# Performance work log

Measured on AMD Instinct MI355X. Metric: run time of the kernel, lower is better.

The kernel has to match this reference:

```python
import jax, jax.numpy as jnp
import numpy as np

V, B, T, H, L = 32000, 32, 128, 512, 2


def setup_inputs() -> dict:
    key = jax.random.key(0)
    k0, k1, k2, k3, k4 = jax.random.split(key, 5)
    return {
        "input_data": jax.random.randint(k0, (B, T), 0, V),
        "targets": jax.random.randint(k1, (B, T), 0, V),
        # tf.random_uniform([vocab, rnn_size], -1, 1)
        "embedding": jax.random.uniform(k2, (V, H), jnp.float32, -1.0, 1.0),
        # one fused gate weight per layer: [concat(x,h)=2H, 4H], gate order i,j,f,o
        "lstm_w": jax.random.normal(k3, (L, 2 * H, 4 * H), jnp.float32) * 0.05,
        "lstm_b": jnp.zeros((L, 4 * H), jnp.float32),
        # truncated_normal(stddev=1/sqrt(rnn_size)) approximated by normal
        "softmax_w": jax.random.normal(k4, (H, V), jnp.float32) / np.sqrt(H),
        "softmax_b": jnp.zeros((V,), jnp.float32),
    }


def _lstm_forward(x_emb, lstm_w, lstm_b):
    # x_emb: [B, T, H]; stacked BasicLSTMCell, forget_bias=0.0, zero initial state
    n_layers = lstm_w.shape[0]
    Bn, Tn, Hn = x_emb.shape
    c0 = jnp.zeros((n_layers, Bn, Hn), x_emb.dtype)
    h0 = jnp.zeros((n_layers, Bn, Hn), x_emb.dtype)

    def step(carry, x_t):
        c, h = carry
        inp = x_t  # [B, H]
        new_c, new_h = [], []
        for l in range(n_layers):  # small fixed structural loop
            gates = jnp.concatenate([inp, h[l]], axis=-1) @ lstm_w[l] + lstm_b[l]
            i, j, f, o = jnp.split(gates, 4, axis=-1)  # TF gate order
            nc = c[l] * jax.nn.sigmoid(f) + jax.nn.sigmoid(i) * jnp.tanh(j)
            nh = jnp.tanh(nc) * jax.nn.sigmoid(o)
            new_c.append(nc)
            new_h.append(nh)
            inp = nh
        return (jnp.stack(new_c), jnp.stack(new_h)), inp

    _, outs = jax.lax.scan(step, (c0, h0), jnp.swapaxes(x_emb, 0, 1))  # [T, B, H]
    return jnp.swapaxes(outs, 0, 1)  # [B, T, H]


def reference(input_data, targets, embedding, lstm_w, lstm_b, softmax_w, softmax_b):
    x = embedding[input_data]  # [B, T, H] gather
    h = _lstm_forward(x, lstm_w, lstm_b)
    logits = h.reshape(-1, h.shape[-1]) @ softmax_w + softmax_b  # [B*T, V]
    logp = jax.nn.log_softmax(logits, axis=-1)
    tflat = targets.reshape(-1)
    loss = -jnp.take_along_axis(logp, tflat[:, None], axis=1)[:, 0]  # per-example CE
    cost = jnp.mean(loss)
    return logits, cost
```

## Files before the change

### kernel.cpp

```cpp
#include <hip/hip_runtime.h>
#include <math.h>

#define VV 32000
#define BB 32
#define TT 128
#define HH 512
#define G4 2048
#define BTT 4096

typedef unsigned short u16;
typedef __attribute__((ext_vector_type(8))) short short8;
typedef __attribute__((ext_vector_type(4))) float f32x4;

static __device__ __forceinline__ float sigm(float x) { return 1.0f / (1.0f + expf(-x)); }

static __device__ __forceinline__ void bsplit(float v, u16& h, u16& l) {
    unsigned u = __float_as_uint(v);
    h = (u16)((u + 0x7FFFu + ((u >> 16) & 1u)) >> 16);
    float vh = __uint_as_float(((unsigned)h) << 16);
    unsigned u2 = __float_as_uint(v - vh);
    l = (u16)((u2 + 0x7FFFu + ((u2 >> 16) & 1u)) >> 16);
}

static __device__ __forceinline__ void gl_lds16(const void* g, void* l) {
    __builtin_amdgcn_global_load_lds(
        (const __attribute__((address_space(1))) void*)g,
        (__attribute__((address_space(3))) void*)l, 16, 0, 0);
}

__global__ void k_gather_split(const int* __restrict__ idx, const float* __restrict__ emb,
                               u16* __restrict__ hi, u16* __restrict__ lo) {
    int row = blockIdx.x;
    int e = idx[row];
    float4 v = ((const float4*)(emb + (size_t)e * HH))[threadIdx.x];
    ushort4 h4, l4;
    bsplit(v.x, h4.x, l4.x); bsplit(v.y, h4.y, l4.y);
    bsplit(v.z, h4.z, l4.z); bsplit(v.w, h4.w, l4.w);
    size_t o = (size_t)row * HH + threadIdx.x * 4;
    *(ushort4*)(hi + o) = h4;
    *(ushort4*)(lo + o) = l4;
}

__global__ void k_split4(const float* __restrict__ x, u16* __restrict__ hi,
                         u16* __restrict__ lo, int n4) {
    int i = blockIdx.x * 256 + threadIdx.x;
    if (i >= n4) return;
    float4 v = ((const float4*)x)[i];
    ushort4 h4, l4;
    bsplit(v.x, h4.x, l4.x); bsplit(v.y, h4.y, l4.y);
    bsplit(v.z, h4.z, l4.z); bsplit(v.w, h4.w, l4.w);
    *(ushort4*)(hi + (size_t)i * 4) = h4;
    *(ushort4*)(lo + (size_t)i * 4) = l4;
}

__global__ void k_zero(float* __restrict__ p, int n) {
    int i = blockIdx.x * blockDim.x + threadIdx.x;
    if (i < n) p[i] = 0.0f;
}

__global__ void k_transposeN(const float* __restrict__ src, float* __restrict__ dst, int K) {
    int gc = blockIdx.x;
    float* d = dst + (size_t)gc * K;
    for (int k = threadIdx.x; k < K; k += blockDim.x)
        d[k] = src[(size_t)k * G4 + gc];
}

__global__ __launch_bounds__(256) void k_tsplit(const float* __restrict__ src,
                                                u16* __restrict__ dhi, u16* __restrict__ dlo,
                                                int K, int N) {
    __shared__ float t[32][33];
    int kb = blockIdx.y << 5, nb = blockIdx.x << 5;
    int r = threadIdx.x >> 5, c = threadIdx.x & 31;
    #pragma unroll
    for (int it = 0; it < 4; ++it)
        t[it * 8 + r][c] = src[(size_t)(kb + it * 8 + r) * N + nb + c];
    __syncthreads();
    #pragma unroll
    for (int it = 0; it < 4; ++it) {
        int n = nb + it * 8 + r, k = kb + c;
        u16 h, l;
        bsplit(t[c][it * 8 + r], h, l);
        dhi[(size_t)n * K + k] = h;
        dlo[(size_t)n * K + k] = l;
    }
}

__global__ __launch_bounds__(256) void k_mgemm(const u16* __restrict__ Ah, const u16* __restrict__ Al,
                                               const u16* __restrict__ Bh, const u16* __restrict__ Bl,
                                               const float* __restrict__ bias, float* __restrict__ C,
                                               int N, int K) {
    __shared__ u16 lds[4][4096];
    const int tid = threadIdx.x;
    const int lane = tid & 63, wid = tid >> 6;
    const int wm = wid >> 1, wn = wid & 1;
    const int lm = lane & 15, kg = lane >> 4;
    const size_t mbase = (size_t)blockIdx.y * 128, nbase = (size_t)blockIdx.x * 128;

    f32x4 acc[4][4] = {};

    const int q = wid * 128 + lane;
    for (int k0 = 0; k0 < K; k0 += 32) {
        __syncthreads();
        #pragma unroll
        for (int i = 0; i < 2; ++i) {
            int qq = q + i * 64;
            int kgs = qq >> 7, ms = qq & 127;
            size_t ga = (mbase + ms) * K + k0 + kgs * 8;
            size_t gb = (nbase + ms) * K + k0 + kgs * 8;
            int lb_ = (wid * 2 + i) * 512;
            gl_lds16(Ah + ga, &lds[0][lb_]);
            gl_lds16(Al + ga, &lds[1][lb_]);
            gl_lds16(Bh + gb, &lds[2][lb_]);
            gl_lds16(Bl + gb, &lds[3][lb_]);
        }
        __syncthreads();

        short8 ah[4], al[4], bh[4], bl[4];
        const int abase = (kg * 128 + wm * 64 + lm) * 8;
        const int bbase = (kg * 128 + wn * 64 + lm) * 8;
        #pragma unroll
        for (int f = 0; f < 4; ++f) {
            ah[f] = *(const short8*)&lds[0][abase + f * 128];
            al[f] = *(const short8*)&lds[1][abase + f * 128];
            bh[f] = *(const short8*)&lds[2][bbase + f * 128];
            bl[f] = *(const short8*)&lds[3][bbase + f * 128];
        }
        #pragma unroll
        for (int fm = 0; fm < 4; ++fm)
            #pragma unroll
            for (int fn = 0; fn < 4; ++fn) {
                acc[fm][fn] = __builtin_amdgcn_mfma_f32_16x16x32_bf16(ah[fm], bh[fn], acc[fm][fn], 0, 0, 0);
                acc[fm][fn] = __builtin_amdgcn_mfma_f32_16x16x32_bf16(ah[fm], bl[fn], acc[fm][fn], 0, 0, 0);
                acc[fm][fn] = __builtin_amdgcn_mfma_f32_16x16x32_bf16(al[fm], bh[fn], acc[fm][fn], 0, 0, 0);
            }
    }

    float bv[4];
    #pragma unroll
    for (int fn = 0; fn < 4; ++fn) bv[fn] = bias[nbase + wn * 64 + fn * 16 + lm];
    #pragma unroll
    for (int fm = 0; fm < 4; ++fm) {
        size_t row0 = mbase + wm * 64 + fm * 16 + kg * 4;
        #pragma unroll
        for (int fn = 0; fn < 4; ++fn) {
            size_t col = nbase + wn * 64 + fn * 16 + lm;
            #pragma unroll
            for (int r = 0; r < 4; ++r)
                C[(row0 + r) * N + col] = acc[fm][fn][r] + bv[fn];
        }
    }
}

__global__ __launch_bounds__(256) void k_stepP(const float* __restrict__ wt1,
                                               const float* __restrict__ wt2,
                                               const float* __restrict__ xg1,
                                               const float* __restrict__ lb2,
                                               float* __restrict__ st,
                                               float* __restrict__ hall1,
                                               float* __restrict__ hall2,
                                               int s) {
    __shared__ float gs[512];
    float* h1buf[2] = {st, st + 16384};
    float* c1 = st + 2 * 16384;
    float* h2buf[2] = {st + 3 * 16384, st + 4 * 16384};
    float* c2 = st + 5 * 16384;
    const int tid = threadIdx.x;

    if (blockIdx.x < 128) {
        int t = s;
        if (t >= TT) return;
        const int cg = blockIdx.x >> 1;
        const int bg = blockIdx.x & 1;
        const float* hp = h1buf[t & 1];
        float* hn = h1buf[(t & 1) ^ 1];
        const int b = tid >> 4, g = (tid >> 2) & 3, ch2 = tid & 3;
        const int batch = bg * 16 + b;
        const int gc0 = g * HH + cg * 8 + ch2;
        const float4* w0 = (const float4*)(wt1 + (size_t)gc0 * HH);
        const float4* w1 = (const float4*)(wt1 + (size_t)(gc0 + 4) * HH);
        const float4* hr = (const float4*)(hp + batch * HH);
        float a0 = 0.f, a1 = 0.f;
        #pragma unroll 4
        for (int i = 0; i < HH / 4; ++i) {
            float4 h4 = hr[i], x0 = w0[i], x1 = w1[i];
            a0 += x0.x * h4.x + x0.y * h4.y + x0.z * h4.z + x0.w * h4.w;
            a1 += x1.x * h4.x + x1.y * h4.y + x1.z * h4.z + x1.w * h4.w;
        }
        size_t xrow = ((size_t)batch * TT + t) * G4;
        gs[(b * 4 + g) * 8 + ch2]     = a0 + xg1[xrow + gc0];
        gs[(b * 4 + g) * 8 + ch2 + 4] = a1 + xg1[xrow + gc0 + 4];
        __syncthreads();
        if (tid < 128) {
            int bb = tid >> 3, cc = tid & 7;
            int batch2 = bg * 16 + bb, chan = cg * 8 + cc;
            float gi = gs[(bb * 4 + 0) * 8 + cc], gj = gs[(bb * 4 + 1) * 8 + cc];
            float gf = gs[(bb * 4 + 2) * 8 + cc], go = gs[(bb * 4 + 3) * 8 + cc];
            size_t ci = (size_t)batch2 * HH + chan;
            float nc = c1[ci] * sigm(gf) + sigm(gi) * tanhf(gj);
            float nh = tanhf(nc) * sigm(go);
            c1[ci] = nc;
            hn[ci] = nh;
            hall1[((size_t)batch2 * TT + t) * HH + chan] = nh;
        }
    } else {
        int tt = s - 1;
        if (tt < 0) return;
        const int idx = blockIdx.x - 128;
        const int cg = idx >> 2;
        const int bg = idx & 3;
        const float* hp = h2buf[tt & 1];
        float* hn = h2buf[(tt & 1) ^ 1];
        const int b = tid >> 5, g = (tid >> 3) & 3, ch = tid & 7;
        const int batch = bg * 8 + b;
        const int gc = g * HH + cg * 8 + ch;
        const float4* wx = (const float4*)(wt2 + (size_t)gc * 1024);
        const float4* wh = wx + HH / 4;
        const float4* xr = (const float4*)(hall1 + ((size_t)batch * TT + tt) * HH);
        const float4* hr = (const float4*)(hp + batch * HH);
        float a = 0.f;
        #pragma unroll 4
        for (int i = 0; i < HH / 4; ++i) {
            float4 x4 = xr[i], w4 = wx[i];
            a += w4.x * x4.x + w4.y * x4.y + w4.z * x4.z + w4.w * x4.w;
        }
        #pragma unroll 4
        for (int i = 0; i < HH / 4; ++i) {
            float4 h4 = hr[i], w4 = wh[i];
            a += w4.x * h4.x + w4.y * h4.y + w4.z * h4.z + w4.w * h4.w;
        }
        gs[(b * 4 + g) * 8 + ch] = a + lb2[gc];
        __syncthreads();
        if (tid < 64) {
            int bb = tid >> 3, cc = tid & 7;
            int batch2 = bg * 8 + bb, chan = cg * 8 + cc;
            float gi = gs[(bb * 4 + 0) * 8 + cc], gj = gs[(bb * 4 + 1) * 8 + cc];
            float gf = gs[(bb * 4 + 2) * 8 + cc], go = gs[(bb * 4 + 3) * 8 + cc];
            size_t ci = (size_t)batch2 * HH + chan;
            float nc = c2[ci] * sigm(gf) + sigm(gi) * tanhf(gj);
            float nh = tanhf(nc) * sigm(go);
            c2[ci] = nc;
            hn[ci] = nh;
            hall2[((size_t)batch2 * TT + tt) * HH + chan] = nh;
        }
    }
}

__global__ __launch_bounds__(256) void k_loss(const float* __restrict__ logits,
                                              const int* __restrict__ tgt,
                                              float* __restrict__ rowloss) {
    int row = blockIdx.x;
    const float* lr = logits + (size_t)row * VV;
    float m = -INFINITY, s = 0.f;
    for (int c = threadIdx.x; c < VV; c += 256) {
        float x = lr[c];
        if (x > m) { s = s * __expf(m - x) + 1.f; m = x; }
        else       { s += __expf(x - m); }
    }
    #pragma unroll
    for (int off = 32; off > 0; off >>= 1) {
        float mo = __shfl_down(m, off);
        float so = __shfl_down(s, off);
        if (mo > m) { s = s * __expf(m - mo) + so; m = mo; }
        else        { s += so * __expf(mo - m); }
    }
    __shared__ float sm[4], ss[4];
    int wid = threadIdx.x >> 6;
    if ((threadIdx.x & 63) == 0) { sm[wid] = m; ss[wid] = s; }
    __syncthreads();
    if (threadIdx.x == 0) {
        m = sm[0]; s = ss[0];
        for (int w = 1; w < 4; ++w) {
            float mo = sm[w], so = ss[w];
            if (mo > m) { s = s * __expf(m - mo) + so; m = mo; }
            else        { s += so * __expf(mo - m); }
        }
        float tl = lr[tgt[row]];
        rowloss[row] = -(tl - m - logf(s));
    }
}

__global__ void k_meanloss(const float* __restrict__ rowloss, float* __restrict__ out) {
    float s = 0.f;
    for (int i = threadIdx.x; i < BTT; i += 256) s += rowloss[i];
    #pragma unroll
    for (int off = 32; off > 0; off >>= 1) s += __shfl_down(s, off);
    __shared__ float wsum[4];
    int wid = threadIdx.x >> 6;
    if ((threadIdx.x & 63) == 0) wsum[wid] = s;
    __syncthreads();
    if (threadIdx.x == 0) out[0] = (wsum[0] + wsum[1] + wsum[2] + wsum[3]) * (1.0f / BTT);
}

extern "C" void kernel_launch(void* const* d_in, const int* in_sizes, int n_in,
                              void* d_out, int out_size, void* d_ws, size_t ws_size,
                              hipStream_t stream) {
    const int*   ids = (const int*)d_in[0];
    const int*   tgt = (const int*)d_in[1];
    const float* emb = (const float*)d_in[2];
    const float* lw  = (const float*)d_in[3];
    const float* lb  = (const float*)d_in[4];
    const float* sw  = (const float*)d_in[5];
    const float* sb  = (const float*)d_in[6];
    float* logits = (float*)d_out;
    float* cost   = logits + (size_t)BTT * VV;

    float* hall1 = (float*)d_ws;
    float* hall2 = hall1 + 2097152;
    float* xgbuf = hall2 + 2097152;
    float* wt1   = xgbuf + 8388608;
    float* wt2   = wt1 + 1048576;
    float* stt   = wt2 + 2097152;
    float* rloss = stt + 98304;
    u16* xa_hi  = (u16*)(rloss + 4096);
    u16* xa_lo  = xa_hi + (size_t)BTT * HH;
    u16* wxt_hi = xa_lo + (size_t)BTT * HH;
    u16* wxt_lo = wxt_hi + (size_t)G4 * HH;
    u16* swt_hi = wxt_lo + (size_t)G4 * HH;
    u16* swt_lo = swt_hi + (size_t)VV * HH;

    k_transposeN<<<G4, 128, 0, stream>>>(lw + (size_t)HH * G4, wt1, HH);
    k_transposeN<<<G4, 128, 0, stream>>>(lw + (size_t)2 * HH * G4, wt2, 2 * HH);
    {
        dim3 gt(G4 / 32, HH / 32);
        k_tsplit<<<gt, 256, 0, stream>>>(lw, wxt_hi, wxt_lo, HH, G4);
    }
    {
        dim3 gt(VV / 32, HH / 32);
        k_tsplit<<<gt, 256, 0, stream>>>(sw, swt_hi, swt_lo, HH, VV);
    }
    k_gather_split<<<BTT, 128, 0, stream>>>(ids, emb, xa_hi, xa_lo);
    k_zero<<<(98304 + 255) / 256, 256, 0, stream>>>(stt, 98304);

    dim3 gg(G4 / 128, BTT / 128);
    k_mgemm<<<gg, 256, 0, stream>>>(xa_hi, xa_lo, wxt_hi, wxt_lo, lb, xgbuf, G4, HH);

    for (int s = 0; s <= TT; ++s)
        k_stepP<<<384, 256, 0, stream>>>(wt1, wt2, xgbuf, lb + G4, stt, hall1, hall2, s);

    k_split4<<<(BTT * HH / 4 + 255) / 256, 256, 0, stream>>>(hall2, xa_hi, xa_lo, BTT * HH / 4);
    dim3 gp(VV / 128, BTT / 128);
    k_mgemm<<<gp, 256, 0, stream>>>(xa_hi, xa_lo, swt_hi, swt_lo, sb, logits, VV, HH);
    k_loss<<<BTT, 256, 0, stream>>>(logits, tgt, rloss);
    k_meanloss<<<1, 256, 0, stream>>>(rloss, cost);
}
```

Measured before the change: 10.18 ms.

## Replace per-timestep LSTM launches with persistent kernel using global atomic barriers

Swaps the 129 per-step kernel launches for one persistent kernel of 384 workgroups. Each layer's workgroups loop over all timesteps, keep cell state in registers and sync through global atomic counters with spin-wait barriers, and layer 2 waits on layer 1's counter to pipeline the two layers. Hidden states move to a [T,B,H] layout and a new split kernel reorders them for the projection GEMM. This removes launch and state-memory overhead, but it relies on all workgroups being co-resident and adds spin-barrier latency at every step.

After: 18.06 ms. 77.3% more time.

```diff
diff --git a/kernel.cpp b/kernel.cpp
--- a/kernel.cpp
+++ b/kernel.cpp
@@ -8,6 +8,10 @@
 #define G4 2048
 #define BTT 4096
 
+#define L1_WGS 128
+#define L2_WGS 256
+#define NWG (L1_WGS + L2_WGS)
+
 typedef unsigned short u16;
 typedef __attribute__((ext_vector_type(8))) short short8;
 typedef __attribute__((ext_vector_type(4))) float f32x4;
@@ -26,6 +30,10 @@
     __builtin_amdgcn_global_load_lds(
         (const __attribute__((address_space(1))) void*)g,
         (__attribute__((address_space(3))) void*)l, 16, 0, 0);
+}
+
+static __device__ __forceinline__ unsigned aload(const unsigned* p) {
+    return __hip_atomic_load(p, __ATOMIC_RELAXED, __HIP_MEMORY_SCOPE_AGENT);
 }
 
 __global__ void k_gather_split(const int* __restrict__ idx, const float* __restrict__ emb,
@@ -41,21 +49,9 @@
     *(ushort4*)(lo + o) = l4;
 }
 
-__global__ void k_split4(const float* __restrict__ x, u16* __restrict__ hi,
-                         u16* __restrict__ lo, int n4) {
-    int i = blockIdx.x * 256 + threadIdx.x;
-    if (i >= n4) return;
-    float4 v = ((const float4*)x)[i];
-    ushort4 h4, l4;
-    bsplit(v.x, h4.x, l4.x); bsplit(v.y, h4.y, l4.y);
-    bsplit(v.z, h4.z, l4.z); bsplit(v.w, h4.w, l4.w);
-    *(ushort4*)(hi + (size_t)i * 4) = h4;
-    *(ushort4*)(lo + (size_t)i * 4) = l4;
-}
-
-__global__ void k_zero(float* __restrict__ p, int n) {
+__global__ void k_zero(unsigned* __restrict__ p, int n) {
     int i = blockIdx.x * blockDim.x + threadIdx.x;
-    if (i < n) p[i] = 0.0f;
+    if (i < n) p[i] = 0u;
 }
 
 __global__ void k_transposeN(const float* __restrict__ src, float* __restrict__ dst, int K) {
@@ -151,98 +147,120 @@
     }
 }
 
-__global__ __launch_bounds__(256) void k_stepP(const float* __restrict__ wt1,
-                                               const float* __restrict__ wt2,
-                                               const float* __restrict__ xg1,
-                                               const float* __restrict__ lb2,
-                                               float* __restrict__ st,
-                                               float* __restrict__ hall1,
-                                               float* __restrict__ hall2,
-                                               int s) {
-    __shared__ float gs[512];
-    float* h1buf[2] = {st, st + 16384};
-    float* c1 = st + 2 * 16384;
-    float* h2buf[2] = {st + 3 * 16384, st + 4 * 16384};
-    float* c2 = st + 5 * 16384;
+__global__ __launch_bounds__(256, 2) void k_lstm(const float* __restrict__ wt1,
+                                                 const float* __restrict__ wt2,
+                                                 const float* __restrict__ xg1,
+                                                 const float* __restrict__ lb2,
+                                                 float* __restrict__ hall1,
+                                                 float* __restrict__ hall2,
+                                                 unsigned* __restrict__ sync) {
+    __shared__ float gs[4][4][32];
     const int tid = threadIdx.x;
-
-    if (blockIdx.x < 128) {
-        int t = s;
-        if (t >= TT) return;
-        const int cg = blockIdx.x >> 1;
-        const int bg = blockIdx.x & 1;
-        const float* hp = h1buf[t & 1];
-        float* hn = h1buf[(t & 1) ^ 1];
-        const int b = tid >> 4, g = (tid >> 2) & 3, ch2 = tid & 3;
-        const int batch = bg * 16 + b;
-        const int gc0 = g * HH + cg * 8 + ch2;
-        const float4* w0 = (const float4*)(wt1 + (size_t)gc0 * HH);
-        const float4* w1 = (const float4*)(wt1 + (size_t)(gc0 + 4) * HH);
-        const float4* hr = (const float4*)(hp + batch * HH);
-        float a0 = 0.f, a1 = 0.f;
-        #pragma unroll 4
-        for (int i = 0; i < HH / 4; ++i) {
-            float4 h4 = hr[i], x0 = w0[i], x1 = w1[i];
-            a0 += x0.x * h4.x + x0.y * h4.y + x0.z * h4.z + x0.w * h4.w;
-            a1 += x1.x * h4.x + x1.y * h4.y + x1.z * h4.z + x1.w * h4.w;
-        }
-        size_t xrow = ((size_t)batch * TT + t) * G4;
-        gs[(b * 4 + g) * 8 + ch2]     = a0 + xg1[xrow + gc0];
-        gs[(b * 4 + g) * 8 + ch2 + 4] = a1 + xg1[xrow + gc0 + 4];
-        __syncthreads();
-        if (tid < 128) {
-            int bb = tid >> 3, cc = tid & 7;
-            int batch2 = bg * 16 + bb, chan = cg * 8 + cc;
-            float gi = gs[(bb * 4 + 0) * 8 + cc], gj = gs[(bb * 4 + 1) * 8 + cc];
-            float gf = gs[(bb * 4 + 2) * 8 + cc], go = gs[(bb * 4 + 3) * 8 + cc];
-            size_t ci = (size_t)batch2 * HH + chan;
-            float nc = c1[ci] * sigm(gf) + sigm(gi) * tanhf(gj);
-            float nh = tanhf(nc) * sigm(go);
-            c1[ci] = nc;
-            hn[ci] = nh;
-            hall1[((size_t)batch2 * TT + t) * HH + chan] = nh;
+    const int b = tid & 31;
+
+    if (blockIdx.x < L1_WGS) {
+        const int cl = tid >> 6, half = (tid >> 5) & 1;
+        const int chan = blockIdx.x * 4 + cl;
+        const float4* w0 = (const float4*)(wt1 + (size_t)((half * 2 + 0) * HH + chan) * HH);
+        const float4* w1 = (const float4*)(wt1 + (size_t)((half * 2 + 1) * HH + chan) * HH);
+        float c_reg = 0.f;
+        for (int s = 0; s < TT; ++s) {
+            size_t xrow = ((size_t)b * TT + s) * G4;
+            float a0 = xg1[xrow + (half * 2 + 0) * HH + chan];
+            float a1 = xg1[xrow + (half * 2 + 1) * HH + chan];
+            if (s > 0) {
+                const float4* inp = (const float4*)(hall1 + ((size_t)(s - 1) * BB + b) * HH);
+                #pragma unroll 4
+                for (int k = 0; k < HH / 4; ++k) {
+                    float4 x4 = inp[k], p4 = w0[k], q4 = w1[k];
+                    a0 += p4.x * x4.x + p4.y * x4.y + p4.z * x4.z + p4.w * x4.w;
+                    a1 += q4.x * x4.x + q4.y * x4.y + q4.z * x4.z + q4.w * x4.w;
+                }
+            }
+            if (half == 0) gs[cl][0][b] = sigm(a0) * tanhf(a1);
+            else         { gs[cl][2][b] = sigm(a0); gs[cl][3][b] = sigm(a1); }
+            __syncthreads();
+            if (half == 0) {
+                float nc = c_reg * gs[cl][2][b] + gs[cl][0][b];
+                float nh = tanhf(nc) * gs[cl][3][b];
+                c_reg = nc;
+                hall1[((size_t)s * BB + b) * HH + chan] = nh;
+            }
+            __threadfence();
+            __syncthreads();
+            if (tid == 0) {
+                __hip_atomic_fetch_add(&sync[0], 1u, __ATOMIC_RELAXED, __HIP_MEMORY_SCOPE_AGENT);
+                unsigned it = 0, tgt = (unsigned)(L1_WGS * (s + 1));
+                while (aload(&sync[0]) < tgt && ++it < (1u << 22)) __builtin_amdgcn_s_sleep(2);
+            }
+            __syncthreads();
+            __threadfence();
         }
     } else {
-        int tt = s - 1;
-        if (tt < 0) return;
-        const int idx = blockIdx.x - 128;
-        const int cg = idx >> 2;
-        const int bg = idx & 3;
-        const float* hp = h2buf[tt & 1];
-        float* hn = h2buf[(tt & 1) ^ 1];
-        const int b = tid >> 5, g = (tid >> 3) & 3, ch = tid & 7;
-        const int batch = bg * 8 + b;
-        const int gc = g * HH + cg * 8 + ch;
-        const float4* wx = (const float4*)(wt2 + (size_t)gc * 1024);
+        const int idx = blockIdx.x - L1_WGS;
+        const int cl = tid >> 7, g = (tid >> 5) & 3;
+        const int chan = idx * 2 + cl;
+        const int gcol = g * HH + chan;
+        const float4* wx = (const float4*)(wt2 + (size_t)gcol * 1024);
         const float4* wh = wx + HH / 4;
-        const float4* xr = (const float4*)(hall1 + ((size_t)batch * TT + tt) * HH);
-        const float4* hr = (const float4*)(hp + batch * HH);
-        float a = 0.f;
-        #pragma unroll 4
-        for (int i = 0; i < HH / 4; ++i) {
-            float4 x4 = xr[i], w4 = wx[i];
-            a += w4.x * x4.x + w4.y * x4.y + w4.z * x4.z + w4.w * x4.w;
-        }
-        #pragma unroll 4
-        for (int i = 0; i < HH / 4; ++i) {
-            float4 h4 = hr[i], w4 = wh[i];
-            a += w4.x * h4.x + w4.y * h4.y + w4.z * h4.z + w4.w * h4.w;
-        }
-        gs[(b * 4 + g) * 8 + ch] = a + lb2[gc];
-        __syncthreads();
-        if (tid < 64) {
-            int bb = tid >> 3, cc = tid & 7;
-            int batch2 = bg * 8 + bb, chan = cg * 8 + cc;
-            float gi = gs[(bb * 4 + 0) * 8 + cc], gj = gs[(bb * 4 + 1) * 8 + cc];
-            float gf = gs[(bb * 4 + 2) * 8 + cc], go = gs[(bb * 4 + 3) * 8 + cc];
-            size_t ci = (size_t)batch2 * HH + chan;
-            float nc = c2[ci] * sigm(gf) + sigm(gi) * tanhf(gj);
-            float nh = tanhf(nc) * sigm(go);
-            c2[ci] = nc;
-            hn[ci] = nh;
-            hall2[((size_t)batch2 * TT + tt) * HH + chan] = nh;
-        }
-    }
+        const float bias = lb2[gcol];
+        float c_reg = 0.f;
+        for (int s = 0; s < TT; ++s) {
+            if (tid == 0) {
+                unsigned it = 0, tgt = (unsigned)(L1_WGS * (s + 1));
+                while (aload(&sync[0]) < tgt && ++it < (1u << 22)) __builtin_amdgcn_s_sleep(2);
+            }
+            __syncthreads();
+            __threadfence();
+            float a = bias;
+            {
+                const float4* xin = (const float4*)(hall1 + ((size_t)s * BB + b) * HH);
+                #pragma unroll 4
+                for (int k = 0; k < HH / 4; ++k) {
+                    float4 x4 = xin[k], p4 = wx[k];
+                    a += p4.x * x4.x + p4.y * x4.y + p4.z * x4.z + p4.w * x4.w;
+                }
+            }
+            if (s > 0) {
+                const float4* hin = (const float4*)(hall2 + ((size_t)(s - 1) * BB + b) * HH);
+                #pragma unroll 4
+                for (int k = 0; k < HH / 4; ++k) {
+                    float4 x4 = hin[k], p4 = wh[k];
+                    a += p4.x * x4.x + p4.y * x4.y + p4.z * x4.z + p4.w * x4.w;
+                }
+            }
+            gs[cl][g][b] = (g == 1) ? tanhf(a) : sigm(a);
+            __syncthreads();
+            if (g == 0) {
+                float nc = c_reg * gs[cl][2][b] + gs[cl][0][b] * gs[cl][1][b];
+                float nh = tanhf(nc) * gs[cl][3][b];
+                c_reg = nc;
+                hall2[((size_t)s * BB + b) * HH + chan] = nh;
+            }
+            __threadfence();
+            __syncthreads();
+            if (tid == 0) {
+                __hip_atomic_fetch_add(&sync[1], 1u, __ATOMIC_RELAXED, __HIP_MEMORY_SCOPE_AGENT);
+                unsigned it = 0, tgt = (unsigned)(L2_WGS * (s + 1));
+                while (aload(&sync[1]) < tgt && ++it < (1u << 22)) __builtin_amdgcn_s_sleep(2);
+            }
+            __syncthreads();
+            __threadfence();
+        }
+    }
+}
+
+__global__ void k_splitTB(const float* __restrict__ hall2, u16* __restrict__ hi,
+                          u16* __restrict__ lo) {
+    int r = blockIdx.x;
+    int bb = r >> 7, t = r & (TT - 1);
+    float4 v = ((const float4*)(hall2 + ((size_t)t * BB + bb) * HH))[threadIdx.x];
+    ushort4 h4, l4;
+    bsplit(v.x, h4.x, l4.x); bsplit(v.y, h4.y, l4.y);
+    bsplit(v.z, h4.z, l4.z); bsplit(v.w, h4.w, l4.w);
+    size_t o = (size_t)r * HH + threadIdx.x * 4;
+    *(ushort4*)(hi + o) = h4;
+    *(ushort4*)(lo + o) = l4;
 }
 
 __global__ __launch_bounds__(256) void k_loss(const float* __restrict__ logits,
@@ -309,9 +327,9 @@
     float* xgbuf = hall2 + 2097152;
     float* wt1   = xgbuf + 8388608;
     float* wt2   = wt1 + 1048576;
-    float* stt   = wt2 + 2097152;
-    float* rloss = stt + 98304;
-    u16* xa_hi  = (u16*)(rloss + 4096);
+    float* rloss = wt2 + 2097152;
+    unsigned* syncv = (unsigned*)(rloss + 4096);
+    u16* xa_hi  = (u16*)(syncv + 16);
     u16* xa_lo  = xa_hi + (size_t)BTT * HH;
     u16* wxt_hi = xa_lo + (size_t)BTT * HH;
     u16* wxt_lo = wxt_hi + (size_t)G4 * HH;
@@ -329,15 +347,14 @@
         k_tsplit<<<gt, 256, 0, stream>>>(sw, swt_hi, swt_lo, HH, VV);
     }
     k_gather_split<<<BTT, 128, 0, stream>>>(ids, emb, xa_hi, xa_lo);
-    k_zero<<<(98304 + 255) / 256, 256, 0, stream>>>(stt, 98304);
+    k_zero<<<1, 64, 0, stream>>>(syncv, 16);
 
     dim3 gg(G4 / 128, BTT / 128);
     k_mgemm<<<gg, 256, 0, stream>>>(xa_hi, xa_lo, wxt_hi, wxt_lo, lb, xgbuf, G4, HH);
 
-    for (int s = 0; s <= TT; ++s)
-        k_stepP<<<384, 256, 0, stream>>>(wt1, wt2, xgbuf, lb + G4, stt, hall1, hall2, s);
-
-    k_split4<<<(BTT * HH / 4 + 255) / 256, 256, 0, stream>>>(hall2, xa_hi, xa_lo, BTT * HH / 4);
+    k_lstm<<<NWG, 256, 0, stream>>>(wt1, wt2, xgbuf, lb + G4, hall1, hall2, syncv);
+
+    k_splitTB<<<BTT, 128, 0, stream>>>(hall2, xa_hi, xa_lo);
     dim3 gp(VV / 128, BTT / 128);
     k_mgemm<<<gp, 256, 0, stream>>>(xa_hi, xa_lo, swt_hi, swt_lo, sb, logits, VV, HH);
     k_loss<<<BTT, 256, 0, stream>>>(logits, tgt, rloss);
```
